# Kernel optimization log

Hardware: AMD Instinct MI355X
Metric: run time of the kernel (lower is better)

The kernel has to match this reference:

```python
import jax, jax.numpy as jnp
import numpy as np
from jax import lax

T, B, H, W, C = 256, 64, 7, 7, 3
HID = 128
HIST = 16
EMB = 128  # conv output channels; 7->4->2->1 spatial, so embed dim = 128


def setup_inputs() -> dict:
    key = jax.random.key(0)
    ks = jax.random.split(key, 16)
    s = 0.05
    inp = {
        "inputs": jax.random.normal(ks[0], (T, B, H, W, C), jnp.float32),
        "done": jax.random.bernoulli(ks[1], 0.05, (T, B)),
        # conv feature extractor (OIHW)
        "conv1_w": jax.random.normal(ks[2], (32, 3, 3, 3), jnp.float32) * s,
        "conv1_b": jnp.zeros((32,), jnp.float32),
        "conv2_w": jax.random.normal(ks[3], (32, 32, 3, 3), jnp.float32) * s,
        "conv2_b": jnp.zeros((32,), jnp.float32),
        "conv3_w": jax.random.normal(ks[4], (EMB, 32, 3, 3), jnp.float32) * s,
        "conv3_b": jnp.zeros((EMB,), jnp.float32),
        # readin: Linear(128 -> HID)
        "readin_w": jax.random.normal(ks[5], (HID, EMB), jnp.float32) * s,
        "readin_b": jnp.zeros((HID,), jnp.float32),
        # LSTMCell(HID, HID)
        "w_ih": jax.random.normal(ks[6], (4 * HID, HID), jnp.float32) * s,
        "w_hh": jax.random.normal(ks[7], (4 * HID, HID), jnp.float32) * s,
        "b_ih": jnp.zeros((4 * HID,), jnp.float32),
        "b_hh": jnp.zeros((4 * HID,), jnp.float32),
        # readout: Linear(HID -> 128)
        "readout_w": jax.random.normal(ks[8], (EMB, HID), jnp.float32) * s,
        "readout_b": jnp.zeros((EMB,), jnp.float32),
    }
    return inp


def _conv(x, w, b):
    # stride 2, padding 1, NCHW / OIHW
    y = lax.conv_general_dilated(x, w, (2, 2), [(1, 1), (1, 1)],
                                 dimension_numbers=("NCHW", "OIHW", "NCHW"))
    return y + b[None, :, None, None]


def _pad_unfold(x, hist):
    # x: [T, B, C] -> [hist, T*B, C]; contexts[h, t] = padded_x[t + h]
    xp = jnp.pad(x, ((hist - 1, 0), (0, 0), (0, 0)))
    ctx = jnp.stack([xp[h:h + x.shape[0]] for h in range(hist)], axis=0)
    return ctx.reshape(hist, x.shape[0] * x.shape[1], x.shape[2])


def reference(inputs, done, conv1_w, conv1_b, conv2_w, conv2_b, conv3_w, conv3_b,
              readin_w, readin_b, w_ih, w_hh, b_ih, b_hh, readout_w, readout_b):
    # --- embed (MinigridStateEmbeddingNet) ---
    x = inputs.reshape(T * B, H, W, C).astype(jnp.float32)
    x = jnp.transpose(x, (0, 3, 2, 1))  # torch transpose(1,3): [TB, C, W, H]
    x = jax.nn.elu(_conv(x, conv1_w, conv1_b))
    x = jax.nn.elu(_conv(x, conv2_w, conv2_b))
    x = jax.nn.elu(_conv(x, conv3_w, conv3_b))
    x = x.reshape(T, B, -1)  # [T, B, 128]

    # --- readin ---
    x = x @ readin_w.T + readin_b  # [T, B, HID]

    # --- pad_unfold over time history ---
    ctx = _pad_unfold(x, HIST)                               # [HIST, T*B, HID]
    d = done[:, :, None]                                     # [T, B, 1] bool
    dctx = _pad_unfold(d, HIST)                              # [HIST, T*B, 1]

    # --- run_sequence: LSTM scan with done-masked resets ---
    def lstm_step(xt, h, c):
        gates = xt @ w_ih.T + b_ih + h @ w_hh.T + b_hh
        i, f, g, o = jnp.split(gates, 4, axis=-1)
        c2 = jax.nn.sigmoid(f) * c + jax.nn.sigmoid(i) * jnp.tanh(g)
        h2 = jax.nn.sigmoid(o) * jnp.tanh(c2)
        return h2, c2

    zeros = jnp.zeros((T * B, HID), jnp.float32)
    h1, c1 = lstm_step(ctx[0], zeros, zeros)

    def step(carry, xd):
        h, c = carry
        xt, dt = xd
        h = jnp.where(dt, 0.0, h)
        c = jnp.where(dt, 0.0, c)
        h, c = lstm_step(xt, h, c)
        return (h, c), h

    _, hs = lax.scan(step, (h1, c1), (ctx[1:], dctx[1:]))
    outputs = jnp.concatenate([h1[None], hs], axis=0)        # [HIST, T*B, HID]

    # --- readout, take last history step ---
    out = outputs @ readout_w.T + readout_b                  # [HIST, T*B, 128]
    out = out.reshape(HIST, T, B, EMB)[-1]                   # [T, B, 128]
    return out
```

## Files before the change

### kernel.cpp

```cpp
#include <hip/hip_runtime.h>

typedef _Float16 half8 __attribute__((ext_vector_type(8)));
typedef _Float16 half4 __attribute__((ext_vector_type(4)));
typedef float f32x4 __attribute__((ext_vector_type(4)));

__device__ __forceinline__ float eluf(float x)   { return x > 0.f ? x : __expf(x) - 1.f; }
__device__ __forceinline__ float sigf(float x) {
  return __builtin_amdgcn_rcpf(1.f + __expf(-x));
}
__device__ __forceinline__ float tanhff(float x) {
  return 1.f - 2.f * __builtin_amdgcn_rcpf(__expf(2.f * x) + 1.f);
}

__device__ __forceinline__ half8 cvt8(const float* __restrict__ p) {
  f32x4 v0 = *(const f32x4*)p;
  f32x4 v1 = *(const f32x4*)(p + 4);
  half8 r;
  r[0] = (_Float16)v0[0]; r[1] = (_Float16)v0[1]; r[2] = (_Float16)v0[2]; r[3] = (_Float16)v0[3];
  r[4] = (_Float16)v1[0]; r[5] = (_Float16)v1[1]; r[6] = (_Float16)v1[2]; r[7] = (_Float16)v1[3];
  return r;
}
#define MFMA(a, b, c) __builtin_amdgcn_mfma_f32_16x16x32_f16(a, b, c, 0, 0, 0)

__global__ __launch_bounds__(256) void k_done(const unsigned char* __restrict__ raw,
                                              unsigned long long* __restrict__ dmask) {
  __shared__ int f0, f1;
  if (threadIdx.x == 0) { f0 = 0; f1 = 0; }
  __syncthreads();
  int l0 = 0, l1 = 0;
  for (int i = threadIdx.x; i < 16384; i += 256)
    if (raw[i]) { if (i & 3) l0 = 1; else l1 = 1; }
  if (l0) atomicOr(&f0, 1);
  if (l1) atomicOr(&f1, 1);
  __syncthreads();
  int mode = (f0 && f1) ? 0 : (f1 ? 1 : (f0 ? 2 : 0));
  const int t = blockIdx.x;
  if (threadIdx.x < 64) {
    int i = t * 64 + threadIdx.x;
    bool v;
    if (mode == 0)      v = raw[i] != 0;
    else if (mode == 1) v = ((const int*)raw)[i] != 0;
    else                v = (((const float*)raw)[i] != 0.f);
    unsigned long long m = __ballot(v);
    if (threadIdx.x == 0) dmask[t] = m;
  }
}

__global__ __launch_bounds__(512, 3) void k_conv(
    const float* __restrict__ inp,
    const float* __restrict__ c1w, const float* __restrict__ c1b,
    const float* __restrict__ c2w, const float* __restrict__ c2b,
    const float* __restrict__ c3w, const float* __restrict__ c3b,
    const float* __restrict__ riw, const float* __restrict__ rib,
    const float* __restrict__ wih, const float* __restrict__ bih,
    const float* __restrict__ bhh,
    _Float16* __restrict__ xgh)
{
  extern __shared__ char L[];
  unsigned*  LUT32 = (unsigned*)L;
  _Float16*  ic1   = (_Float16*)(L + 128);
  _Float16*  a1t   = (_Float16*)(L + 16512);
  _Float16*  a2    = (_Float16*)(L + 53632);
  _Float16*  ft    = (_Float16*)(L + 128);
  _Float16*  yb    = (_Float16*)(L + 8320);

  const int tid  = threadIdx.x;
  const int lane = tid & 63;
  const int wv   = tid >> 6;
  const int lr   = lane & 15;
  const int lg   = lane >> 4;
  const int t    = blockIdx.x >> 1;
  const int bh   = blockIdx.x & 1;

  const int ntl  = wv & 1;
  const int mq   = wv >> 1;
  const int o1   = ntl * 16 + lr;

  if (tid < 32) {
    unsigned v = 0xFFFFFFFFu;
    if (tid < 27) { int c = tid / 9, r9 = tid % 9; v = (unsigned)(c | ((r9 / 3) << 8) | ((r9 % 3) << 16)); }
    LUT32[tid] = v;
  }

  half8 B1;
  #pragma unroll
  for (int e = 0; e < 8; ++e) {
    int k = lg * 8 + e;
    B1[e] = (_Float16)((k < 27) ? c1w[o1 * 27 + k] : 0.f);
  }
  const float b1o = c1b[o1];

  half8 B2t[9];
  {
    const float* base = c2w + o1 * 288 + lg * 72;
    #pragma unroll
    for (int h = 0; h < 2; ++h) {
      float buf[36];
      #pragma unroll
      for (int v = 0; v < 9; ++v)
        *(f32x4*)(buf + v * 4) = *(const f32x4*)(base + h * 36 + v * 4);
      #pragma unroll
      for (int tap = 0; tap < 9; ++tap)
        #pragma unroll
        for (int e2 = 0; e2 < 4; ++e2)
          B2t[tap][h * 4 + e2] = (_Float16)buf[e2 * 9 + tap];
    }
  }
  const float b2o = c2b[o1];

  for (int ch = 0; ch < 2; ++ch) {
    __syncthreads();
    for (int i = tid; i < 18560 / 2; i += 512) ((unsigned*)a1t)[i] = 0u;
    {
      const size_t n0 = (size_t)(t * 64 + bh * 32 + ch * 16) * 147;
      #pragma unroll
      for (int j = 0; j < 16; ++j) {
        int e = tid + j * 512;
        int row = e >> 5, k = e & 31;
        int s = row >> 4, pos = row & 15;
        int p = pos >> 2, q = pos & 3;
        unsigned lut = LUT32[k];
        float v = 0.f;
        if (lut != 0xFFFFFFFFu) {
          int c = lut & 0xFF, dp = (lut >> 8) & 0xFF, dq = (lut >> 16) & 0xFF;
          int pp = 2 * p + dp - 1, qq = 2 * q + dq - 1;
          if ((unsigned)pp < 7u && (unsigned)qq < 7u)
            v = inp[n0 + s * 147 + qq * 21 + pp * 3 + c];
        }
        ic1[row * 32 + (k ^ ((row & 3) << 3))] = (_Float16)v;
      }
    }
    __syncthreads();
    #pragma unroll
    for (int mi = 0; mi < 4; ++mi) {
      const int mtile = mq * 4 + mi;
      const int rowA  = mtile * 16 + lr;
      half8 a = *(const half8*)(ic1 + rowA * 32 + ((lg * 8) ^ ((rowA & 3) << 3)));
      f32x4 acc; acc[0] = b1o; acc[1] = b1o; acc[2] = b1o; acc[3] = b1o;
      acc = MFMA(a, B1, acc);
      #pragma unroll
      for (int r = 0; r < 4; ++r) {
        int m1 = mtile * 16 + lg * 4 + r;
        int s = m1 >> 4, pos = m1 & 15;
        int p = pos >> 2, q = pos & 3;
        int xy = (p + 1) * 6 + (q + 1);
        a1t[s * 1160 + xy * 32 + (o1 ^ ((xy & 3) << 3))] = (_Float16)eluf(acc[r]);
      }
    }
    __syncthreads();
    {
      f32x4 acc; acc[0] = b2o; acc[1] = b2o; acc[2] = b2o; acc[3] = b2o;
      const int rowm = mq * 16 + lr;
      const int s2 = rowm >> 2, pos2 = rowm & 3;
      const int p2 = pos2 >> 1, q2 = pos2 & 1;
      #pragma unroll
      for (int tap = 0; tap < 9; ++tap) {
        const int dp = tap / 3, dq = tap % 3;
        const int xy2 = (2 * p2 + dp) * 6 + (2 * q2 + dq);
        half8 a = *(const half8*)(a1t + s2 * 1160 + xy2 * 32 + ((lg * 8) ^ ((xy2 & 3) << 3)));
        acc = MFMA(a, B2t[tap], acc);
      }
      #pragma unroll
      for (int r = 0; r < 4; ++r) {
        int m = mq * 16 + lg * 4 + r;
        int s2w = m >> 2, pos = m & 3;
        int arow = ch * 16 + s2w;
        int col = o1 * 4 + pos;
        a2[arow * 128 + (col ^ ((arow & 7) << 3))] = (_Float16)eluf(acc[r]);
      }
    }
  }
  __syncthreads();

  {
    half8 B3[4];
    #pragma unroll
    for (int kt = 0; kt < 4; ++kt) {
      half8 b;
      #pragma unroll
      for (int e = 0; e < 8; ++e) {
        int k = kt * 32 + lg * 8 + e;
        int i = k >> 2, pos = k & 3;
        int widx = 4 + (pos >> 1) * 3 + (pos & 1);
        b[e] = (_Float16)c3w[(wv * 16 + lr) * 288 + i * 9 + widx];
      }
      B3[kt] = b;
    }
    float bb = c3b[wv * 16 + lr];
    #pragma unroll
    for (int mt = 0; mt < 2; ++mt) {
      f32x4 acc; acc[0] = bb; acc[1] = bb; acc[2] = bb; acc[3] = bb;
      const int row = mt * 16 + lr;
      #pragma unroll
      for (int kt = 0; kt < 4; ++kt) {
        half8 a = *(const half8*)(a2 + row * 128 + ((kt * 32 + lg * 8) ^ ((row & 7) << 3)));
        acc = MFMA(a, B3[kt], acc);
      }
      #pragma unroll
      for (int r = 0; r < 4; ++r) {
        int m = mt * 16 + lg * 4 + r;
        ft[m * 128 + ((wv * 16 + lr) ^ ((m & 7) << 3))] = (_Float16)eluf(acc[r]);
      }
    }
  }
  __syncthreads();

  {
    half8 R1[4];
    #pragma unroll
    for (int kt = 0; kt < 4; ++kt)
      R1[kt] = cvt8(riw + (wv * 16 + lr) * 128 + kt * 32 + lg * 8);
    float bb = rib[wv * 16 + lr];
    #pragma unroll
    for (int mt = 0; mt < 2; ++mt) {
      f32x4 acc; acc[0] = bb; acc[1] = bb; acc[2] = bb; acc[3] = bb;
      const int row = mt * 16 + lr;
      #pragma unroll
      for (int kt = 0; kt < 4; ++kt) {
        half8 a = *(const half8*)(ft + row * 128 + ((kt * 32 + lg * 8) ^ ((row & 7) << 3)));
        acc = MFMA(a, R1[kt], acc);
      }
      #pragma unroll
      for (int r = 0; r < 4; ++r) {
        int m = mt * 16 + lg * 4 + r;
        yb[m * 128 + ((wv * 16 + lr) ^ ((m & 7) << 3))] = (_Float16)acc[r];
      }
    }
  }
  __syncthreads();

  {
    half8 W2f[4][4];
    float bg[4];
    #pragma unroll
    for (int ty = 0; ty < 4; ++ty) {
      int g = ty * 128 + wv * 16 + lr;
      bg[ty] = bih[g] + bhh[g];
      #pragma unroll
      for (int kt = 0; kt < 4; ++kt)
        W2f[kt][ty] = cvt8(wih + g * 128 + kt * 32 + lg * 8);
    }
    #pragma unroll
    for (int mt = 0; mt < 2; ++mt) {
      const int row = mt * 16 + lr;
      half8 a[4];
      #pragma unroll
      for (int kt = 0; kt < 4; ++kt)
        a[kt] = *(const half8*)(yb + row * 128 + ((kt * 32 + lg * 8) ^ ((row & 7) << 3)));
      #pragma unroll
      for (int ty = 0; ty < 4; ++ty) {
        f32x4 acc; acc[0] = bg[ty]; acc[1] = bg[ty]; acc[2] = bg[ty]; acc[3] = bg[ty];
        #pragma unroll
        for (int kt = 0; kt < 4; ++kt) acc = MFMA(a[kt], W2f[kt][ty], acc);
        int g = ty * 128 + wv * 16 + lr;
        half4 h4;
        h4[0] = (_Float16)acc[0]; h4[1] = (_Float16)acc[1];
        h4[2] = (_Float16)acc[2]; h4[3] = (_Float16)acc[3];
        *(half4*)(xgh + ((size_t)t * 512 + g) * 64 + bh * 32 + mt * 16 + lg * 4) = h4;
      }
    }
  }
}

__global__ __launch_bounds__(512, 2) void k_lstm(
    const float* __restrict__ whh, const float* __restrict__ bih,
    const float* __restrict__ bhh, const _Float16* __restrict__ xgh,
    const unsigned long long* __restrict__ dmask,
    const float* __restrict__ row_, const float* __restrict__ rob,
    float* __restrict__ out)
{
  __shared__ _Float16 H[2][32 * 128];

  const int tid  = threadIdx.x;
  const int lane = tid & 63;
  const int wv   = tid >> 6;
  const int lr   = lane & 15, lg = lane >> 4;
  const int xcd  = blockIdx.x & 7;
  const int j    = blockIdx.x >> 3;
  const int t    = (xcd << 5) + (j >> 1);
  const int bh   = j & 1;
  const int bbase = bh * 32;

  half8 Wf[4][4];
  float b0[4];
  #pragma unroll
  for (int ty = 0; ty < 4; ++ty) {
    int g = ty * 128 + wv * 16 + lr;
    b0[ty] = bih[g] + bhh[g];
    #pragma unroll
    for (int kt = 0; kt < 4; ++kt)
      Wf[kt][ty] = cvt8(whh + g * 128 + kt * 32 + lg * 8);
  }

  for (int i = tid; i < 32 * 128 / 2; i += 512) ((unsigned*)H[0])[i] = 0u;

  float cc[2][4];
  #pragma unroll
  for (int mt = 0; mt < 2; ++mt)
    #pragma unroll
    for (int r = 0; r < 4; ++r) cc[mt][r] = 0.f;

  for (int st = 0; st < 16; ++st) {
    const int ts = t + st - 15;
    _Float16* Hr = H[st & 1];
    _Float16* Hw = H[(st & 1) ^ 1];
    __syncthreads();
    const bool hasX = (ts >= 0);
    const unsigned long long wm =
        (st < 15 && ts + 1 >= 0) ? dmask[ts + 1] : 0ULL;
    const _Float16* xb = xgh + (size_t)ts * 32768 + bbase;
    #pragma unroll
    for (int mt = 0; mt < 2; ++mt) {
      const int rowA = mt * 16 + lr;
      half8 afr[4];
      #pragma unroll
      for (int kt = 0; kt < 4; ++kt)
        afr[kt] = *(const half8*)(Hr + rowA * 128 + ((kt * 32 + lg * 8) ^ ((rowA & 7) << 3)));
      f32x4 acc[4];
      if (hasX) {
        #pragma unroll
        for (int ty = 0; ty < 4; ++ty) {
          half4 p = *(const half4*)(xb + (ty * 128 + wv * 16 + lr) * 64 + mt * 16 + lg * 4);
          acc[ty][0] = (float)p[0]; acc[ty][1] = (float)p[1];
          acc[ty][2] = (float)p[2]; acc[ty][3] = (float)p[3];
        }
      } else {
        #pragma unroll
        for (int ty = 0; ty < 4; ++ty) {
          acc[ty][0] = b0[ty]; acc[ty][1] = b0[ty]; acc[ty][2] = b0[ty]; acc[ty][3] = b0[ty];
        }
      }
      __builtin_amdgcn_s_setprio(1);
      #pragma unroll
      for (int ty = 0; ty < 4; ++ty)
        #pragma unroll
        for (int kt = 0; kt < 4; ++kt)
          acc[ty] = MFMA(afr[kt], Wf[kt][ty], acc[ty]);
      __builtin_amdgcn_s_setprio(0);
      const unsigned mnib = (unsigned)(wm >> (bbase + mt * 16 + lg * 4)) & 15u;
      #pragma unroll
      for (int r = 0; r < 4; ++r) {
        const int s_ = mt * 16 + lg * 4 + r;
        const bool d = (mnib >> r) & 1u;
        float iv = sigf(acc[0][r]);
        float fv = sigf(acc[1][r]);
        float gv = tanhff(acc[2][r]);
        float ov = sigf(acc[3][r]);
        float cn = fmaf(fv, cc[mt][r], iv * gv);
        float hn = ov * tanhff(cn);
        cc[mt][r] = d ? 0.f : cn;
        Hw[s_ * 128 + ((wv * 16 + lr) ^ ((s_ & 7) << 3))] = (_Float16)(d ? 0.f : hn);
      }
    }
  }
  __syncthreads();

  half8 R[4];
  #pragma unroll
  for (int kt = 0; kt < 4; ++kt)
    R[kt] = cvt8(row_ + (wv * 16 + lr) * 128 + kt * 32 + lg * 8);
  float rb2 = rob[wv * 16 + lr];
  #pragma unroll
  for (int mt = 0; mt < 2; ++mt) {
    const int row = mt * 16 + lr;
    f32x4 acc; acc[0] = rb2; acc[1] = rb2; acc[2] = rb2; acc[3] = rb2;
    #pragma unroll
    for (int kt = 0; kt < 4; ++kt) {
      half8 a = *(const half8*)(H[0] + row * 128 + ((kt * 32 + lg * 8) ^ ((row & 7) << 3)));
      acc = MFMA(a, R[kt], acc);
    }
    #pragma unroll
    for (int r = 0; r < 4; ++r) {
      int s = mt * 16 + lg * 4 + r;
      out[(size_t)(t * 64 + bbase + s) * 128 + wv * 16 + lr] = acc[r];
    }
  }
}

extern "C" void kernel_launch(void* const* d_in, const int* in_sizes, int n_in,
                              void* d_out, int out_size, void* d_ws, size_t ws_size,
                              hipStream_t stream) {
  const float* inp = (const float*)d_in[0];
  const void*  don = d_in[1];
  const float* c1w = (const float*)d_in[2];
  const float* c1b = (const float*)d_in[3];
  const float* c2w = (const float*)d_in[4];
  const float* c2b = (const float*)d_in[5];
  const float* c3w = (const float*)d_in[6];
  const float* c3b = (const float*)d_in[7];
  const float* riw = (const float*)d_in[8];
  const float* rib = (const float*)d_in[9];
  const float* wih = (const float*)d_in[10];
  const float* whh = (const float*)d_in[11];
  const float* bih = (const float*)d_in[12];
  const float* bhh = (const float*)d_in[13];
  const float* row_ = (const float*)d_in[14];
  const float* rob = (const float*)d_in[15];

  unsigned long long* dmask = (unsigned long long*)d_ws;
  _Float16* xgh = (_Float16*)((char*)d_ws + 16384);

  (void)hipFuncSetAttribute((const void*)k_conv,
                            hipFuncAttributeMaxDynamicSharedMemorySize, 61952);

  k_done<<<256, 256, 0, stream>>>((const unsigned char*)don, dmask);
  k_conv<<<512, 512, 61952, stream>>>(inp, c1w, c1b, c2w, c2b, c3w, c3b,
                                      riw, rib, wih, bih, bhh, xgh);
  k_lstm<<<512, 512, 0, stream>>>(whh, bih, bhh, xgh, dmask, row_, rob,
                                  (float*)d_out);
}
```

Measured before the change: 220.1 us.

## Stage conv2 weights in LDS and stream input weights to cut register pressure

Conv2 weight fragments now sit in shared memory instead of nine half8 registers per lane. The input-to-hidden weights are converted from global memory inside the MFMA loop rather than preloaded into a 16-entry register array. The input gather loop is only partly unrolled, and the launch-bounds occupancy hint rises from 3 to 4 blocks. The goal is fewer VGPRs and more resident waves for the conv kernel. The cost is extra LDS traffic, repeated global weight loads and a larger dynamic shared allocation, which may itself limit how many blocks fit per CU.

New measurement: 208.5 us. -5.3%, faster.

```diff
diff --git a/kernel.cpp b/kernel.cpp
--- a/kernel.cpp
+++ b/kernel.cpp
@@ -46,7 +46,7 @@
   }
 }
 
-__global__ __launch_bounds__(512, 3) void k_conv(
+__global__ __launch_bounds__(512, 4) void k_conv(
     const float* __restrict__ inp,
     const float* __restrict__ c1w, const float* __restrict__ c1b,
     const float* __restrict__ c2w, const float* __restrict__ c2b,
@@ -61,6 +61,7 @@
   _Float16*  ic1   = (_Float16*)(L + 128);
   _Float16*  a1t   = (_Float16*)(L + 16512);
   _Float16*  a2    = (_Float16*)(L + 53632);
+  _Float16*  c2wL  = (_Float16*)(L + 61824);
   _Float16*  ft    = (_Float16*)(L + 128);
   _Float16*  yb    = (_Float16*)(L + 8320);
 
@@ -82,6 +83,16 @@
     LUT32[tid] = v;
   }
 
+  if (tid < 128) {
+    const int o = tid >> 2, lg2 = tid & 3;
+    const float* src = c2w + o * 288 + lg2 * 72;
+    #pragma unroll 4
+    for (int j = 0; j < 72; ++j) {
+      int i = lg2 * 8 + j / 9, tap = j % 9;
+      c2wL[(o * 9 + tap) * 32 + i] = (_Float16)src[j];
+    }
+  }
+
   half8 B1;
   #pragma unroll
   for (int e = 0; e < 8; ++e) {
@@ -89,23 +100,6 @@
     B1[e] = (_Float16)((k < 27) ? c1w[o1 * 27 + k] : 0.f);
   }
   const float b1o = c1b[o1];
-
-  half8 B2t[9];
-  {
-    const float* base = c2w + o1 * 288 + lg * 72;
-    #pragma unroll
-    for (int h = 0; h < 2; ++h) {
-      float buf[36];
-      #pragma unroll
-      for (int v = 0; v < 9; ++v)
-        *(f32x4*)(buf + v * 4) = *(const f32x4*)(base + h * 36 + v * 4);
-      #pragma unroll
-      for (int tap = 0; tap < 9; ++tap)
-        #pragma unroll
-        for (int e2 = 0; e2 < 4; ++e2)
-          B2t[tap][h * 4 + e2] = (_Float16)buf[e2 * 9 + tap];
-    }
-  }
   const float b2o = c2b[o1];
 
   for (int ch = 0; ch < 2; ++ch) {
@@ -113,7 +107,7 @@
     for (int i = tid; i < 18560 / 2; i += 512) ((unsigned*)a1t)[i] = 0u;
     {
       const size_t n0 = (size_t)(t * 64 + bh * 32 + ch * 16) * 147;
-      #pragma unroll
+      #pragma unroll 4
       for (int j = 0; j < 16; ++j) {
         int e = tid + j * 512;
         int row = e >> 5, k = e & 31;
@@ -157,8 +151,9 @@
       for (int tap = 0; tap < 9; ++tap) {
         const int dp = tap / 3, dq = tap % 3;
         const int xy2 = (2 * p2 + dp) * 6 + (2 * q2 + dq);
-        half8 a = *(const half8*)(a1t + s2 * 1160 + xy2 * 32 + ((lg * 8) ^ ((xy2 & 3) << 3)));
-        acc = MFMA(a, B2t[tap], acc);
+        half8 a  = *(const half8*)(a1t + s2 * 1160 + xy2 * 32 + ((lg * 8) ^ ((xy2 & 3) << 3)));
+        half8 b2 = *(const half8*)(c2wL + (o1 * 9 + tap) * 32 + lg * 8);
+        acc = MFMA(a, b2, acc);
       }
       #pragma unroll
       for (int r = 0; r < 4; ++r) {
@@ -230,16 +225,6 @@
   __syncthreads();
 
   {
-    half8 W2f[4][4];
-    float bg[4];
-    #pragma unroll
-    for (int ty = 0; ty < 4; ++ty) {
-      int g = ty * 128 + wv * 16 + lr;
-      bg[ty] = bih[g] + bhh[g];
-      #pragma unroll
-      for (int kt = 0; kt < 4; ++kt)
-        W2f[kt][ty] = cvt8(wih + g * 128 + kt * 32 + lg * 8);
-    }
     #pragma unroll
     for (int mt = 0; mt < 2; ++mt) {
       const int row = mt * 16 + lr;
@@ -249,10 +234,14 @@
         a[kt] = *(const half8*)(yb + row * 128 + ((kt * 32 + lg * 8) ^ ((row & 7) << 3)));
       #pragma unroll
       for (int ty = 0; ty < 4; ++ty) {
-        f32x4 acc; acc[0] = bg[ty]; acc[1] = bg[ty]; acc[2] = bg[ty]; acc[3] = bg[ty];
+        int g = ty * 128 + wv * 16 + lr;
+        float bg = bih[g] + bhh[g];
+        f32x4 acc; acc[0] = bg; acc[1] = bg; acc[2] = bg; acc[3] = bg;
         #pragma unroll
-        for (int kt = 0; kt < 4; ++kt) acc = MFMA(a[kt], W2f[kt][ty], acc);
-        int g = ty * 128 + wv * 16 + lr;
+        for (int kt = 0; kt < 4; ++kt) {
+          half8 w = cvt8(wih + g * 128 + kt * 32 + lg * 8);
+          acc = MFMA(a[kt], w, acc);
+        }
         half4 h4;
         h4[0] = (_Float16)acc[0]; h4[1] = (_Float16)acc[1];
         h4[2] = (_Float16)acc[2]; h4[3] = (_Float16)acc[3];
@@ -401,10 +390,10 @@
   _Float16* xgh = (_Float16*)((char*)d_ws + 16384);
 
   (void)hipFuncSetAttribute((const void*)k_conv,
-                            hipFuncAttributeMaxDynamicSharedMemorySize, 61952);
+                            hipFuncAttributeMaxDynamicSharedMemorySize, 80256);
 
   k_done<<<256, 256, 0, stream>>>((const unsigned char*)don, dmask);
-  k_conv<<<512, 512, 61952, stream>>>(inp, c1w, c1b, c2w, c2b, c3w, c3b,
+  k_conv<<<512, 512, 80256, stream>>>(inp, c1w, c1b, c2w, c2b, c3w, c3b,
                                       riw, rib, wih, bih, bhh, xgh);
   k_lstm<<<512, 512, 0, stream>>>(whh, bih, bhh, xgh, dmask, row_, rob,
                                   (float*)d_out);
```
